# Optimization experiments

Hardware: AMD Instinct MI355X
Metric: run time of the kernel (lower is better)

Reference implementation:

```python
import jax, jax.numpy as jnp
import numpy as np

B, N, C = 32, 512, 768
H = 12
D = C // H
HID = 4 * C
EPS = 1e-5


def layer_norm(x, w, b):
    mu = jnp.mean(x, axis=-1, keepdims=True)
    var = jnp.mean(jnp.square(x - mu), axis=-1, keepdims=True)
    return (x - mu) * jax.lax.rsqrt(var + EPS) * w + b


def setup_inputs() -> dict:
    key = jax.random.key(0)
    ks = jax.random.split(key, 8)
    s_in = 1.0 / np.sqrt(C)
    s_hid = 1.0 / np.sqrt(HID)
    return {
        "x": jax.random.normal(ks[0], (B, N, C), dtype=jnp.float32),
        "ln1_w": jnp.ones((C,), jnp.float32),
        "ln1_b": jnp.zeros((C,), jnp.float32),
        "qkv_w": jax.random.normal(ks[1], (3 * C, C), jnp.float32) * s_in,
        "proj_w": jax.random.normal(ks[2], (C, C), jnp.float32) * s_in,
        "proj_b": jnp.zeros((C,), jnp.float32),
        "ln2_w": jnp.ones((C,), jnp.float32),
        "ln2_b": jnp.zeros((C,), jnp.float32),
        "fc1_w": jax.random.normal(ks[3], (HID, C), jnp.float32) * s_in,
        "fc1_b": jnp.zeros((HID,), jnp.float32),
        "fc2_w": jax.random.normal(ks[4], (C, HID), jnp.float32) * s_hid,
        "fc2_b": jnp.zeros((C,), jnp.float32),
    }


def reference(x, ln1_w, ln1_b, qkv_w, proj_w, proj_b, ln2_w, ln2_b, fc1_w, fc1_b, fc2_w, fc2_b):
    scale = D ** (-0.5)
    # --- attention on norm1(x) ---
    h = layer_norm(x, ln1_w, ln1_b)                       # [B,N,C]
    qkv = jnp.einsum('bnc,fc->bnf', h, qkv_w)             # [B,N,3C] (no bias)
    qkv = qkv.reshape(B, N, 3, H, D).transpose(2, 0, 3, 1, 4)  # [3,B,H,N,D]
    q, k, v = qkv[0], qkv[1], qkv[2]
    attn = jnp.einsum('bhnd,bhmd->bhnm', q, k) * scale    # [B,H,N,N]
    attn = jax.nn.softmax(attn, axis=-1)
    o = jnp.einsum('bhnm,bhmd->bhnd', attn, v)            # [B,H,N,D]
    o = o.transpose(0, 2, 1, 3).reshape(B, N, C)
    o = jnp.einsum('bnc,oc->bno', o, proj_w) + proj_b
    # --- Block quirk: x = attn_out + drop_path(attn_out) == 2*attn_out (eval) ---
    x = o + o
    # --- MLP residual ---
    h2 = layer_norm(x, ln2_w, ln2_b)
    h2 = jnp.einsum('bnc,hc->bnh', h2, fc1_w) + fc1_b
    h2 = jax.nn.gelu(h2, approximate=False)
    h2 = jnp.einsum('bnh,oh->bno', h2, fc2_w) + fc2_b
    return x + h2
```

## Files before the change

### kernel.cpp

```cpp
#include <hip/hip_runtime.h>

#define B_   32
#define N_   512
#define C_   768
#define H_   12
#define D_   64
#define HID_ 3072
#define BN_  (B_*N_)

typedef unsigned short u16;
typedef __attribute__((ext_vector_type(8))) short  short8;
typedef __attribute__((ext_vector_type(4))) float  float4v;

__device__ __forceinline__ u16 f32_to_bf16(float f) {
  unsigned u = __builtin_bit_cast(unsigned, f);
  u += 0x7fffu + ((u >> 16) & 1u);
  return (u16)(u >> 16);
}

__device__ __forceinline__ void load_lds16(const u16* g, u16* l) {
  __builtin_amdgcn_global_load_lds(
      (const __attribute__((address_space(1))) unsigned int*)g,
      (__attribute__((address_space(3))) unsigned int*)l,
      16, 0, 0);
}

__global__ void cast_kernel(const float* __restrict__ src, u16* __restrict__ dst, int n) {
  int i = blockIdx.x * 256 + threadIdx.x;
  if (i < n) dst[i] = f32_to_bf16(src[i]);
}

__global__ __launch_bounds__(256)
void ln_kernel(const float* __restrict__ x, const float* __restrict__ w,
               const float* __restrict__ bias, u16* __restrict__ out) {
  const int row = blockIdx.x;
  const int tid = threadIdx.x;
  const float* xr = x + (size_t)row * C_;
  float v0 = xr[tid], v1 = xr[tid + 256], v2 = xr[tid + 512];
  float s = v0 + v1 + v2;
  float q = v0*v0 + v1*v1 + v2*v2;
#pragma unroll
  for (int off = 1; off < 64; off <<= 1) { s += __shfl_xor(s, off); q += __shfl_xor(q, off); }
  __shared__ float red[8];
  int wave = tid >> 6, lane = tid & 63;
  if (lane == 0) { red[wave] = s; red[4 + wave] = q; }
  __syncthreads();
  s = red[0] + red[1] + red[2] + red[3];
  q = red[4] + red[5] + red[6] + red[7];
  float mean = s * (1.0f / C_);
  float var  = q * (1.0f / C_) - mean * mean;
  float rstd = rsqrtf(var + 1e-5f);
  u16* orow = out + (size_t)row * C_;
  orow[tid]       = f32_to_bf16((v0 - mean) * rstd * w[tid]       + bias[tid]);
  orow[tid + 256] = f32_to_bf16((v1 - mean) * rstd * w[tid + 256] + bias[tid + 256]);
  orow[tid + 512] = f32_to_bf16((v2 - mean) * rstd * w[tid + 512] + bias[tid + 512]);
}

__global__ __launch_bounds__(256)
void transpose_v(const u16* __restrict__ qkv, u16* __restrict__ vt) {
  __shared__ alignas(16) u16 T[64 * 72];
  const int nt = blockIdx.x, bh = blockIdx.y;
  const int b = bh / H_, h = bh % H_;
  const int tid = threadIdx.x;
  const size_t rs3 = 3 * C_;
  const int r = tid >> 2, dc = (tid & 3) * 16;
  const u16* src = qkv + (size_t)(b * N_ + nt * 64 + r) * rs3 + 2 * C_ + h * D_ + dc;
  short8 a0 = *(const short8*)src;
  short8 a1 = *(const short8*)(src + 8);
#pragma unroll
  for (int j = 0; j < 8; j++) T[(dc + j) * 72 + r] = (u16)a0[j];
#pragma unroll
  for (int j = 0; j < 8; j++) T[(dc + 8 + j) * 72 + r] = (u16)a1[j];
  __syncthreads();
  const int d = tid >> 2, nc = (tid & 3) * 16;
  u16* dst = vt + ((size_t)(b * H_ + h) * D_ + d) * N_ + nt * 64 + nc;
  *(short8*)dst       = *(const short8*)&T[d * 72 + nc];
  *(short8*)(dst + 8) = *(const short8*)&T[d * 72 + nc + 8];
}

template <int EPI>
__device__ __forceinline__ void gemm_core(const u16* __restrict__ A, const u16* __restrict__ W,
                                          int N, int K,
                                          const float* __restrict__ bias,
                                          const float* __restrict__ resid,
                                          u16* __restrict__ out_bf, float* __restrict__ out_f) {
  __shared__ alignas(16) u16 As[128 * 64];
  __shared__ alignas(16) u16 Ws[128 * 64];
  const int tid  = threadIdx.x;
  const int wave = tid >> 6;
  const int lane = tid & 63;
  const int quad = lane >> 4;
  const int l15  = lane & 15;

  const int nx    = gridDim.x;
  const int lin   = blockIdx.y * nx + blockIdx.x;
  const int total = nx * gridDim.y;
  const int v     = (lin & 7) * (total >> 3) + (lin >> 3);
  const int m0 = (v / nx) << 7;
  const int n0 = (v % nx) << 7;

  const int wm = (wave >> 1) * 64;
  const int wn = (wave & 1) * 64;

  float4v acc[4][4];
#pragma unroll
  for (int i = 0; i < 4; i++)
#pragma unroll
    for (int j = 0; j < 4; j++) acc[i][j] = (float4v){0.f, 0.f, 0.f, 0.f};

  const int c0   = wave * 4;
  const int srow = lane >> 3;
  const int gcol = ((lane & 7) ^ srow) * 8;
  const u16* Ag[4];
  const u16* Wg[4];
#pragma unroll
  for (int j = 0; j < 4; j++) {
    const int row = (c0 + j) * 8 + srow;
    Ag[j] = A + (size_t)(m0 + row) * K + gcol;
    Wg[j] = W + (size_t)(n0 + row) * K + gcol;
  }

  for (int k0 = 0; k0 < K; k0 += 64) {
    __syncthreads();
#pragma unroll
    for (int j = 0; j < 4; j++) load_lds16(Ag[j] + k0, &As[(c0 + j) * 512]);
#pragma unroll
    for (int j = 0; j < 4; j++) load_lds16(Wg[j] + k0, &Ws[(c0 + j) * 512]);
    __syncthreads();

    short8 af[4][2], bf[4][2];
#pragma unroll
    for (int mi = 0; mi < 4; mi++)
#pragma unroll
      for (int ks = 0; ks < 2; ks++) {
        const int swz = ((ks * 4 + quad) ^ (l15 & 7)) * 8;
        af[mi][ks] = *(const short8*)&As[(wm + mi * 16 + l15) * 64 + swz];
        bf[mi][ks] = *(const short8*)&Ws[(wn + mi * 16 + l15) * 64 + swz];
      }
#pragma unroll
    for (int ks = 0; ks < 2; ks++)
#pragma unroll
      for (int mi = 0; mi < 4; mi++)
#pragma unroll
        for (int ni = 0; ni < 4; ni++)
          acc[mi][ni] = __builtin_amdgcn_mfma_f32_16x16x32_bf16(af[mi][ks], bf[ni][ks], acc[mi][ni], 0, 0, 0);
  }

#pragma unroll
  for (int mi = 0; mi < 4; mi++) {
#pragma unroll
    for (int r = 0; r < 4; r++) {
      const int row = m0 + wm + mi * 16 + quad * 4 + r;
#pragma unroll
      for (int ni = 0; ni < 4; ni++) {
        const int col = n0 + wn + ni * 16 + l15;
        float v2 = acc[mi][ni][r];
        if (EPI == 0) {
          out_bf[(size_t)row * N + col] = f32_to_bf16(v2);
        } else if (EPI == 1) {
          v2 += bias[col];
          v2 = 0.5f * v2 * (1.0f + erff(v2 * 0.70710678118654752f));
          out_bf[(size_t)row * N + col] = f32_to_bf16(v2);
        } else if (EPI == 2) {
          out_f[(size_t)row * N + col] = 2.0f * (v2 + bias[col]);
        } else {
          out_f[(size_t)row * N + col] = v2 + bias[col] + resid[(size_t)row * N + col];
        }
      }
    }
  }
}

__global__ __launch_bounds__(256, 3)
void gemm_qkv(const u16* __restrict__ A, const u16* __restrict__ W, int N, int K,
              u16* __restrict__ out_bf) {
  gemm_core<0>(A, W, N, K, nullptr, nullptr, out_bf, nullptr);
}
__global__ __launch_bounds__(256, 3)
void gemm_proj2x(const u16* __restrict__ A, const u16* __restrict__ W, int N, int K,
                 const float* __restrict__ bias, float* __restrict__ out_f) {
  gemm_core<2>(A, W, N, K, bias, nullptr, nullptr, out_f);
}
__global__ __launch_bounds__(256, 3)
void gemm_fc1gelu(const u16* __restrict__ A, const u16* __restrict__ W, int N, int K,
                  const float* __restrict__ bias, u16* __restrict__ out_bf) {
  gemm_core<1>(A, W, N, K, bias, nullptr, out_bf, nullptr);
}
__global__ __launch_bounds__(256, 3)
void gemm_fc2res(const u16* __restrict__ A, const u16* __restrict__ W, int N, int K,
                 const float* __restrict__ bias, const float* __restrict__ resid,
                 float* __restrict__ out_f) {
  gemm_core<3>(A, W, N, K, bias, resid, nullptr, out_f);
}

__global__ __launch_bounds__(256)
void attn_kernel(const u16* __restrict__ qkv, const u16* __restrict__ vt,
                 u16* __restrict__ o) {
  __shared__ alignas(16) u16 Ks[64 * 64];
  __shared__ alignas(16) u16 Vs[64 * 64];
  __shared__ alignas(16) u16 Ps[8][16 * 64];
  const int tid  = threadIdx.x;
  const int wave = tid >> 6, lane = tid & 63;
  const int quad = lane >> 4, l15 = lane & 15;
  const int lin = blockIdx.x;
  const int bh = lin % 384, qt = lin / 384;
  const int b = bh / H_, h = bh % H_;
  const size_t rs3 = 3 * C_;

  short8 qf[2][2];
#pragma unroll
  for (int st = 0; st < 2; st++) {
    const int qrow = b * N_ + qt * 128 + st * 64 + wave * 16 + l15;
    const u16* qp = qkv + (size_t)qrow * rs3 + h * D_ + quad * 8;
    qf[st][0] = *(const short8*)qp;
    qf[st][1] = *(const short8*)(qp + 32);
  }

  const int srow = lane >> 3;
  const int gcol = ((lane & 7) ^ srow) * 8;
  const int ch0 = wave * 2, ch1 = wave * 2 + 1;
  const u16* kg0 = qkv + (size_t)(b * N_ + ch0 * 8 + srow) * rs3 + C_ + h * D_ + gcol;
  const u16* kg1 = qkv + (size_t)(b * N_ + ch1 * 8 + srow) * rs3 + C_ + h * D_ + gcol;
  const u16* vg0 = vt + ((size_t)bh * D_ + ch0 * 8 + srow) * N_ + gcol;
  const u16* vg1 = vt + ((size_t)bh * D_ + ch1 * 8 + srow) * N_ + gcol;

  float m[2][4], l[2][4];
  float4v oacc[2][4];
#pragma unroll
  for (int st = 0; st < 2; st++)
#pragma unroll
    for (int r = 0; r < 4; r++) { m[st][r] = -1e30f; l[st][r] = 0.f; }
#pragma unroll
  for (int st = 0; st < 2; st++)
#pragma unroll
    for (int ni = 0; ni < 4; ni++) oacc[st][ni] = (float4v){0.f, 0.f, 0.f, 0.f};

  for (int kt = 0; kt < 8; ++kt) {
    __syncthreads();
    load_lds16(kg0 + (size_t)(kt * 64) * rs3, &Ks[ch0 * 512]);
    load_lds16(kg1 + (size_t)(kt * 64) * rs3, &Ks[ch1 * 512]);
    load_lds16(vg0 + kt * 64, &Vs[ch0 * 512]);
    load_lds16(vg1 + kt * 64, &Vs[ch1 * 512]);
    __syncthreads();

    short8 kf[4][2];
#pragma unroll
    for (int ni = 0; ni < 4; ni++)
#pragma unroll
      for (int ks = 0; ks < 2; ks++)
        kf[ni][ks] = *(const short8*)&Ks[(ni * 16 + l15) * 64 + ((ks * 4 + quad) ^ (l15 & 7)) * 8];

#pragma unroll
    for (int st = 0; st < 2; st++) {
      u16* myPs = Ps[wave * 2 + st];
      float4v s[4];
#pragma unroll
      for (int ni = 0; ni < 4; ni++) {
        s[ni] = (float4v){0.f, 0.f, 0.f, 0.f};
        s[ni] = __builtin_amdgcn_mfma_f32_16x16x32_bf16(qf[st][0], kf[ni][0], s[ni], 0, 0, 0);
        s[ni] = __builtin_amdgcn_mfma_f32_16x16x32_bf16(qf[st][1], kf[ni][1], s[ni], 0, 0, 0);
      }

      float mt[4];
#pragma unroll
      for (int r = 0; r < 4; r++)
        mt[r] = 0.125f * fmaxf(fmaxf(s[0][r], s[1][r]), fmaxf(s[2][r], s[3][r]));
#pragma unroll
      for (int off = 1; off < 16; off <<= 1)
#pragma unroll
        for (int r = 0; r < 4; r++) mt[r] = fmaxf(mt[r], __shfl_xor(mt[r], off));

      float alpha[4], mnew[4], rsum[4];
#pragma unroll
      for (int r = 0; r < 4; r++) {
        mnew[r] = fmaxf(m[st][r], mt[r]);
        alpha[r] = __expf(m[st][r] - mnew[r]);
        rsum[r] = 0.f;
      }
#pragma unroll
      for (int ni = 0; ni < 4; ni++)
#pragma unroll
        for (int r = 0; r < 4; r++) {
          float p = __expf(s[ni][r] * 0.125f - mnew[r]);
          rsum[r] += p;
          const int prow = quad * 4 + r;
          const int g = (ni * 2 + (l15 >> 3)) ^ (prow & 7);
          myPs[prow * 64 + g * 8 + (l15 & 7)] = f32_to_bf16(p);
        }
#pragma unroll
      for (int off = 1; off < 16; off <<= 1)
#pragma unroll
        for (int r = 0; r < 4; r++) rsum[r] += __shfl_xor(rsum[r], off);
#pragma unroll
      for (int r = 0; r < 4; r++) { l[st][r] = l[st][r] * alpha[r] + rsum[r]; m[st][r] = mnew[r]; }
#pragma unroll
      for (int ni = 0; ni < 4; ni++)
#pragma unroll
        for (int r = 0; r < 4; r++) oacc[st][ni][r] *= alpha[r];

#pragma unroll
      for (int ks = 0; ks < 2; ks++) {
        const int g = (ks * 4 + quad) ^ (l15 & 7);
        short8 pf = *(const short8*)&myPs[l15 * 64 + g * 8];
#pragma unroll
        for (int ni = 0; ni < 4; ni++) {
          short8 vf = *(const short8*)&Vs[(ni * 16 + l15) * 64 + ((ks * 4 + quad) ^ (l15 & 7)) * 8];
          oacc[st][ni] = __builtin_amdgcn_mfma_f32_16x16x32_bf16(pf, vf, oacc[st][ni], 0, 0, 0);
        }
      }
    }
  }

#pragma unroll
  for (int st = 0; st < 2; st++) {
    float inv[4];
#pragma unroll
    for (int r = 0; r < 4; r++) inv[r] = 1.0f / l[st][r];
#pragma unroll
    for (int ni = 0; ni < 4; ni++)
#pragma unroll
      for (int r = 0; r < 4; r++) {
        int row = b * N_ + qt * 128 + st * 64 + wave * 16 + quad * 4 + r;
        int col = h * D_ + ni * 16 + l15;
        o[(size_t)row * C_ + col] = f32_to_bf16(oacc[st][ni][r] * inv[r]);
      }
  }
}

extern "C" void kernel_launch(void* const* d_in, const int* in_sizes, int n_in,
                              void* d_out, int out_size, void* d_ws, size_t ws_size,
                              hipStream_t stream) {
  const float* x      = (const float*)d_in[0];
  const float* ln1_w  = (const float*)d_in[1];
  const float* ln1_b  = (const float*)d_in[2];
  const float* qkv_w  = (const float*)d_in[3];
  const float* proj_w = (const float*)d_in[4];
  const float* proj_b = (const float*)d_in[5];
  const float* ln2_w  = (const float*)d_in[6];
  const float* ln2_b  = (const float*)d_in[7];
  const float* fc1_w  = (const float*)d_in[8];
  const float* fc1_b  = (const float*)d_in[9];
  const float* fc2_w  = (const float*)d_in[10];
  const float* fc2_b  = (const float*)d_in[11];
  float* out = (float*)d_out;

  char* ws = (char*)d_ws;
  size_t off = 0;
  auto alloc = [&](size_t bytes) { void* p = ws + off; off += (bytes + 255) & ~255ull; return p; };
  u16* wqkv  = (u16*)alloc((size_t)3 * C_ * C_ * 2);
  u16* wproj = (u16*)alloc((size_t)C_ * C_ * 2);
  u16* wfc1  = (u16*)alloc((size_t)HID_ * C_ * 2);
  u16* wfc2  = (u16*)alloc((size_t)C_ * HID_ * 2);
  u16* regionA = (u16*)alloc((size_t)BN_ * HID_ * 2);
  float* xnew  = (float*)alloc((size_t)BN_ * C_ * 4);
  u16* h2      = (u16*)alloc((size_t)BN_ * C_ * 2);

  u16* hbuf = regionA;
  u16* qkvb = regionA + (size_t)BN_ * C_;
  u16* obuf = regionA;
  u16* act  = regionA;
  u16* vtbuf = (u16*)xnew;

  cast_kernel<<<dim3(3 * C_ * C_ / 256), 256, 0, stream>>>(qkv_w, wqkv, 3 * C_ * C_);
  cast_kernel<<<dim3(C_ * C_ / 256), 256, 0, stream>>>(proj_w, wproj, C_ * C_);
  cast_kernel<<<dim3(HID_ * C_ / 256), 256, 0, stream>>>(fc1_w, wfc1, HID_ * C_);
  cast_kernel<<<dim3(HID_ * C_ / 256), 256, 0, stream>>>(fc2_w, wfc2, C_ * HID_);

  ln_kernel<<<dim3(BN_), 256, 0, stream>>>(x, ln1_w, ln1_b, hbuf);

  gemm_qkv<<<dim3(3 * C_ / 128, BN_ / 128), 256, 0, stream>>>(hbuf, wqkv, 3 * C_, C_, qkvb);

  transpose_v<<<dim3(N_ / 64, B_ * H_), 256, 0, stream>>>(qkvb, vtbuf);

  attn_kernel<<<dim3((N_ / 128) * B_ * H_), 256, 0, stream>>>(qkvb, vtbuf, obuf);

  gemm_proj2x<<<dim3(C_ / 128, BN_ / 128), 256, 0, stream>>>(obuf, wproj, C_, C_, proj_b, xnew);

  ln_kernel<<<dim3(BN_), 256, 0, stream>>>(xnew, ln2_w, ln2_b, h2);

  gemm_fc1gelu<<<dim3(HID_ / 128, BN_ / 128), 256, 0, stream>>>(h2, wfc1, HID_, C_, fc1_b, act);

  gemm_fc2res<<<dim3(C_ / 128, BN_ / 128), 256, 0, stream>>>(act, wfc2, C_, HID_, fc2_b, xnew, out);
}
```

Before: 555.8 us.

## Use 256x128 GEMM tiles for QKV/fc1, tanh GELU, fuse weight casts

Adds a 256x128-tile GEMM core with 8x4 MFMA accumulators per wave for the QKV and fc1 projections, doubling A-tile reuse against the weight tile and halving the grid. The fc1 epilogue switches from erf-based GELU to a tanh approximation computed with a fast exp. The four weight cast launches are merged into one kernel. The larger tile raises LDS and register use and lowers occupancy, and the GELU approximation adds small numerical error.

```diff
diff --git a/kernel.cpp b/kernel.cpp
--- a/kernel.cpp
+++ b/kernel.cpp
@@ -18,6 +18,11 @@
   return (u16)(u >> 16);
 }
 
+__device__ __forceinline__ float gelu_tanh(float x) {
+  float z2 = 1.5957691216f * (x + 0.044715f * x * x * x);
+  return x - x / (__expf(z2) + 1.0f);
+}
+
 __device__ __forceinline__ void load_lds16(const u16* g, u16* l) {
   __builtin_amdgcn_global_load_lds(
       (const __attribute__((address_space(1))) unsigned int*)g,
@@ -25,9 +30,17 @@
       16, 0, 0);
 }
 
-__global__ void cast_kernel(const float* __restrict__ src, u16* __restrict__ dst, int n) {
+__global__ __launch_bounds__(256)
+void cast_all_kernel(const float* __restrict__ qkv_w, const float* __restrict__ proj_w,
+                     const float* __restrict__ fc1_w, const float* __restrict__ fc2_w,
+                     u16* __restrict__ wqkv, u16* __restrict__ wproj,
+                     u16* __restrict__ wfc1, u16* __restrict__ wfc2) {
+  const int n1 = 3 * C_ * C_, n2 = n1 + C_ * C_, n3 = n2 + HID_ * C_;
   int i = blockIdx.x * 256 + threadIdx.x;
-  if (i < n) dst[i] = f32_to_bf16(src[i]);
+  if (i < n1)       wqkv[i]       = f32_to_bf16(qkv_w[i]);
+  else if (i < n2)  wproj[i - n1] = f32_to_bf16(proj_w[i - n1]);
+  else if (i < n3)  wfc1[i - n2]  = f32_to_bf16(fc1_w[i - n2]);
+  else              wfc2[i - n3]  = f32_to_bf16(fc2_w[i - n3]);
 }
 
 __global__ __launch_bounds__(256)
@@ -79,18 +92,107 @@
 }
 
 template <int EPI>
+__device__ __forceinline__ void gemm256_core(const u16* __restrict__ A, const u16* __restrict__ W,
+                                             int N, int K, const float* __restrict__ bias,
+                                             u16* __restrict__ out_bf) {
+  __shared__ alignas(16) u16 As[256 * 64];
+  __shared__ alignas(16) u16 Ws[128 * 64];
+  const int tid  = threadIdx.x;
+  const int wave = tid >> 6, lane = tid & 63;
+  const int quad = lane >> 4, l15 = lane & 15;
+
+  const int nx    = gridDim.x;
+  const int lin   = blockIdx.y * nx + blockIdx.x;
+  const int total = nx * gridDim.y;
+  const int v     = (lin & 7) * (total >> 3) + (lin >> 3);
+  const int m0 = (v / nx) << 8;
+  const int n0 = (v % nx) << 7;
+
+  const int wm = (wave >> 1) << 7;
+  const int wn = (wave & 1) << 6;
+
+  float4v acc[8][4];
+#pragma unroll
+  for (int i = 0; i < 8; i++)
+#pragma unroll
+    for (int j = 0; j < 4; j++) acc[i][j] = (float4v){0.f, 0.f, 0.f, 0.f};
+
+  const int srow = lane >> 3;
+  const int gcol = ((lane & 7) ^ srow) * 8;
+  const u16* Ag[8];
+  const u16* Wg[4];
+#pragma unroll
+  for (int j = 0; j < 8; j++)
+    Ag[j] = A + (size_t)(m0 + (wave * 8 + j) * 8 + srow) * K + gcol;
+#pragma unroll
+  for (int j = 0; j < 4; j++)
+    Wg[j] = W + (size_t)(n0 + (wave * 4 + j) * 8 + srow) * K + gcol;
+
+  for (int k0 = 0; k0 < K; k0 += 64) {
+    __syncthreads();
+#pragma unroll
+    for (int j = 0; j < 8; j++) load_lds16(Ag[j] + k0, &As[(wave * 8 + j) * 512]);
+#pragma unroll
+    for (int j = 0; j < 4; j++) load_lds16(Wg[j] + k0, &Ws[(wave * 4 + j) * 512]);
+    __syncthreads();
+
+#pragma unroll
+    for (int ks = 0; ks < 2; ks++) {
+      const int swz = ((ks * 4 + quad) ^ (l15 & 7)) * 8;
+      short8 af[8], bf[4];
+#pragma unroll
+      for (int mi = 0; mi < 8; mi++) af[mi] = *(const short8*)&As[(wm + mi * 16 + l15) * 64 + swz];
+#pragma unroll
+      for (int ni = 0; ni < 4; ni++) bf[ni] = *(const short8*)&Ws[(wn + ni * 16 + l15) * 64 + swz];
+#pragma unroll
+      for (int mi = 0; mi < 8; mi++)
+#pragma unroll
+        for (int ni = 0; ni < 4; ni++)
+          acc[mi][ni] = __builtin_amdgcn_mfma_f32_16x16x32_bf16(af[mi], bf[ni], acc[mi][ni], 0, 0, 0);
+    }
+  }
+
+#pragma unroll
+  for (int mi = 0; mi < 8; mi++) {
+#pragma unroll
+    for (int r = 0; r < 4; r++) {
+      const int row = m0 + wm + mi * 16 + quad * 4 + r;
+#pragma unroll
+      for (int ni = 0; ni < 4; ni++) {
+        const int col = n0 + wn + ni * 16 + l15;
+        float v2 = acc[mi][ni][r];
+        if (EPI == 0) {
+          out_bf[(size_t)row * N + col] = f32_to_bf16(v2);
+        } else {
+          out_bf[(size_t)row * N + col] = f32_to_bf16(gelu_tanh(v2 + bias[col]));
+        }
+      }
+    }
+  }
+}
+
+__global__ __launch_bounds__(256, 2)
+void gemm_qkv(const u16* __restrict__ A, const u16* __restrict__ W, int N, int K,
+              u16* __restrict__ out_bf) {
+  gemm256_core<0>(A, W, N, K, nullptr, out_bf);
+}
+__global__ __launch_bounds__(256, 2)
+void gemm_fc1gelu(const u16* __restrict__ A, const u16* __restrict__ W, int N, int K,
+                  const float* __restrict__ bias, u16* __restrict__ out_bf) {
+  gemm256_core<1>(A, W, N, K, bias, out_bf);
+}
+
+template <int EPI>
 __device__ __forceinline__ void gemm_core(const u16* __restrict__ A, const u16* __restrict__ W,
                                           int N, int K,
                                           const float* __restrict__ bias,
                                           const float* __restrict__ resid,
-                                          u16* __restrict__ out_bf, float* __restrict__ out_f) {
+                                          float* __restrict__ out_f) {
   __shared__ alignas(16) u16 As[128 * 64];
   __shared__ alignas(16) u16 Ws[128 * 64];
   const int tid  = threadIdx.x;
-  const int wave = tid >> 6;
-  const int lane = tid & 63;
-  const int quad = lane >> 4;
-  const int l15  = lane & 15;
+  const int wave = tid >> 6, lane = tid & 63;
+  const int quad = lane >> 4, l15 = lane & 15;
 
   const int nx    = gridDim.x;
   const int lin   = blockIdx.y * nx + blockIdx.x;
@@ -155,13 +257,7 @@
       for (int ni = 0; ni < 4; ni++) {
         const int col = n0 + wn + ni * 16 + l15;
         float v2 = acc[mi][ni][r];
-        if (EPI == 0) {
-          out_bf[(size_t)row * N + col] = f32_to_bf16(v2);
-        } else if (EPI == 1) {
-          v2 += bias[col];
-          v2 = 0.5f * v2 * (1.0f + erff(v2 * 0.70710678118654752f));
-          out_bf[(size_t)row * N + col] = f32_to_bf16(v2);
-        } else if (EPI == 2) {
+        if (EPI == 2) {
           out_f[(size_t)row * N + col] = 2.0f * (v2 + bias[col]);
         } else {
           out_f[(size_t)row * N + col] = v2 + bias[col] + resid[(size_t)row * N + col];
@@ -172,25 +268,15 @@
 }
 
 __global__ __launch_bounds__(256, 3)
-void gemm_qkv(const u16* __restrict__ A, const u16* __restrict__ W, int N, int K,
-              u16* __restrict__ out_bf) {
-  gemm_core<0>(A, W, N, K, nullptr, nullptr, out_bf, nullptr);
-}
-__global__ __launch_bounds__(256, 3)
 void gemm_proj2x(const u16* __restrict__ A, const u16* __restrict__ W, int N, int K,
                  const float* __restrict__ bias, float* __restrict__ out_f) {
-  gemm_core<2>(A, W, N, K, bias, nullptr, nullptr, out_f);
-}
-__global__ __launch_bounds__(256, 3)
-void gemm_fc1gelu(const u16* __restrict__ A, const u16* __restrict__ W, int N, int K,
-                  const float* __restrict__ bias, u16* __restrict__ out_bf) {
-  gemm_core<1>(A, W, N, K, bias, nullptr, out_bf, nullptr);
+  gemm_core<2>(A, W, N, K, bias, nullptr, out_f);
 }
 __global__ __launch_bounds__(256, 3)
 void gemm_fc2res(const u16* __restrict__ A, const u16* __restrict__ W, int N, int K,
                  const float* __restrict__ bias, const float* __restrict__ resid,
                  float* __restrict__ out_f) {
-  gemm_core<3>(A, W, N, K, bias, resid, nullptr, out_f);
+  gemm_core<3>(A, W, N, K, bias, resid, out_f);
 }
 
 __global__ __launch_bounds__(256)
@@ -361,14 +447,13 @@
   u16* act  = regionA;
   u16* vtbuf = (u16*)xnew;
 
-  cast_kernel<<<dim3(3 * C_ * C_ / 256), 256, 0, stream>>>(qkv_w, wqkv, 3 * C_ * C_);
-  cast_kernel<<<dim3(C_ * C_ / 256), 256, 0, stream>>>(proj_w, wproj, C_ * C_);
-  cast_kernel<<<dim3(HID_ * C_ / 256), 256, 0, stream>>>(fc1_w, wfc1, HID_ * C_);
-  cast_kernel<<<dim3(HID_ * C_ / 256), 256, 0, stream>>>(fc2_w, wfc2, C_ * HID_);
+  const int ncast = (3 * C_ * C_ + C_ * C_ + HID_ * C_ + C_ * HID_) / 256;
+  cast_all_kernel<<<dim3(ncast), 256, 0, stream>>>(qkv_w, proj_w, fc1_w, fc2_w,
+                                                   wqkv, wproj, wfc1, wfc2);
 
   ln_kernel<<<dim3(BN_), 256, 0, stream>>>(x, ln1_w, ln1_b, hbuf);
 
-  gemm_qkv<<<dim3(3 * C_ / 128, BN_ / 128), 256, 0, stream>>>(hbuf, wqkv, 3 * C_, C_, qkvb);
+  gemm_qkv<<<dim3(3 * C_ / 128, BN_ / 256), 256, 0, stream>>>(hbuf, wqkv, 3 * C_, C_, qkvb);
 
   transpose_v<<<dim3(N_ / 64, B_ * H_), 256, 0, stream>>>(qkvb, vtbuf);
 
@@ -378,7 +463,7 @@
 
   ln_kernel<<<dim3(BN_), 256, 0, stream>>>(xnew, ln2_w, ln2_b, h2);
 
-  gemm_fc1gelu<<<dim3(HID_ / 128, BN_ / 128), 256, 0, stream>>>(h2, wfc1, HID_, C_, fc1_b, act);
+  gemm_fc1gelu<<<dim3(HID_ / 128, BN_ / 256), 256, 0, stream>>>(h2, wfc1, HID_, C_, fc1_b, act);
 
   gemm_fc2res<<<dim3(C_ / 128, BN_ / 128), 256, 0, stream>>>(act, wfc2, C_, HID_, fc2_b, xnew, out);
 }
```

Result: no change. 556.1 us (+0.1%).
